# Performance work log

Measured on AMD Instinct MI355X. Metric: run time of the kernel, lower is better.

## Reference

```python
import jax, jax.numpy as jnp
import numpy as np

# dims matching init_kwargs
U, T, S, K = 2048, 200, 10, 20   # users, history_length, slate_size, num_topics
DE, DU, V, H = 32, 32, 100000, 16  # doc_embed_dim, user_embed_dim, num_docs, rnn hidden
D_IN = DE + (S + 1) + (S + 1) * K + 1  # 264 concatenated feature width
LEAKY_ALPHA = 0.3  # keras LeakyReLU default


def setup_inputs() -> dict:
    key = jax.random.key(0)
    ks = jax.random.split(key, 9)
    slate_doc_quality_history = jax.random.normal(ks[0], (U, T, S), jnp.float32)
    slate_doc_features_history = jax.random.normal(ks[1], (U, T, S, K), jnp.float32)
    docid_history = jax.random.randint(ks[2], (U, T), 0, V + 1)  # 0 is the masked id
    ctime_history = jax.random.uniform(ks[3], (U, T), jnp.float32)
    # learned parameters
    emb_table = jax.random.normal(ks[4], (V + 1, DE), jnp.float32) * 0.05
    Wx = jax.random.normal(ks[5], (D_IN, H), jnp.float32) * (1.0 / np.sqrt(D_IN))
    Wh = jax.random.normal(ks[6], (H, H), jnp.float32) * (1.0 / np.sqrt(H))
    b_rnn = jnp.zeros((H,), jnp.float32)
    Wd = jax.random.normal(ks[7], (H, DU), jnp.float32) * (1.0 / np.sqrt(H))
    b_dense = jnp.zeros((DU,), jnp.float32)
    return dict(
        slate_doc_quality_history=slate_doc_quality_history,
        slate_doc_features_history=slate_doc_features_history,
        docid_history=docid_history,
        ctime_history=ctime_history,
        emb_table=emb_table, Wx=Wx, Wh=Wh, b_rnn=b_rnn, Wd=Wd, b_dense=b_dense,
    )


def reference(slate_doc_quality_history, slate_doc_features_history, docid_history,
              ctime_history, emb_table, Wx, Wh, b_rnn, Wd, b_dense):
    B, Tlen = docid_history.shape
    # embedding lookup; mask_zero=True -> timesteps with id==0 are skipped by the RNN
    emb = emb_table[docid_history]                                   # [U,T,DE]
    mask = docid_history != 0                                        # [U,T]
    # append zero quality column -> [U,T,S+1]
    q = jnp.concatenate([slate_doc_quality_history,
                         jnp.zeros((B, Tlen, 1), slate_doc_quality_history.dtype)], axis=-1)
    # append zero feature row on slate axis, flatten -> [U,T,(S+1)*K]
    f = jnp.concatenate([slate_doc_features_history,
                         jnp.zeros((B, Tlen, 1, K), slate_doc_features_history.dtype)], axis=-2)
    f = f.reshape(B, Tlen, -1)
    x = jnp.concatenate([emb, q, f, ctime_history[..., None]], axis=-1)  # [U,T,D_IN]

    # SimpleRNN(16): h_t = tanh(x_t Wx + h_{t-1} Wh + b); masked steps keep previous h
    pre = jnp.einsum('btd,dh->bth', x, Wx) + b_rnn                   # [U,T,H]

    def step(h, inp):
        pre_t, m_t = inp                                             # [U,H], [U]
        h_new = jnp.tanh(pre_t + h @ Wh)
        h = jnp.where(m_t[:, None], h_new, h)
        return h, None

    h0 = jnp.zeros((B, Wh.shape[0]), x.dtype)
    hT, _ = jax.lax.scan(step, h0, (pre.transpose(1, 0, 2), mask.T))
    # LeakyReLU(alpha=0.3) then Dense -> user embeddings [U, DU]
    a = jnp.where(hT >= 0, hT, LEAKY_ALPHA * hT)
    return a @ Wd + b_dense
```

## Files before the change

kernel.cpp:

```cpp
#include <hip/hip_runtime.h>

#define U_   2048
#define T_   200
#define S_   10
#define K_   20
#define H_   16
#define DU_  32
#define DE_  32
#define DIN_ 264

__global__ __launch_bounds__(256) void k_pre(
    const float* __restrict__ q, const float* __restrict__ f,
    const int* __restrict__ docid, const float* __restrict__ ct,
    const float* __restrict__ emb, const float* __restrict__ Wx,
    const float* __restrict__ brnn, float* __restrict__ pre)
{
    const int idx = blockIdx.x * 256 + threadIdx.x;

    float acc[H_];
#pragma unroll
    for (int h = 0; h < H_; ++h) acc[h] = brnn[h];

    {
        const float4* f4 = (const float4*)(f + (size_t)idx * (S_ * K_));
#pragma unroll 5
        for (int r = 0; r < (S_ * K_) / 4; ++r) {
            float4 v = f4[r];
            const float* w = Wx + (DE_ + S_ + 1 + r * 4) * H_;
#pragma unroll
            for (int h = 0; h < H_; ++h)
                acc[h] += v.x * w[h] + v.y * w[h + 16] + v.z * w[h + 32] + v.w * w[h + 48];
        }
    }

    {
        const float4* e4 = (const float4*)(emb + (size_t)docid[idx] * DE_);
#pragma unroll
        for (int r = 0; r < DE_ / 4; ++r) {
            float4 v = e4[r];
            const float* w = Wx + (r * 4) * H_;
#pragma unroll
            for (int h = 0; h < H_; ++h)
                acc[h] += v.x * w[h] + v.y * w[h + 16] + v.z * w[h + 32] + v.w * w[h + 48];
        }
    }

    {
        const float2* q2 = (const float2*)(q + (size_t)idx * S_);
#pragma unroll
        for (int r = 0; r < S_ / 2; ++r) {
            float2 v = q2[r];
            const float* w = Wx + (DE_ + r * 2) * H_;
#pragma unroll
            for (int h = 0; h < H_; ++h)
                acc[h] += v.x * w[h] + v.y * w[h + 16];
        }
    }

    {
        float c = ct[idx];
        const float* w = Wx + (DIN_ - 1) * H_;
#pragma unroll
        for (int h = 0; h < H_; ++h) acc[h] += c * w[h];
    }

    float4* o = (float4*)(pre + (size_t)idx * H_);
    o[0] = make_float4(acc[0], acc[1], acc[2], acc[3]);
    o[1] = make_float4(acc[4], acc[5], acc[6], acc[7]);
    o[2] = make_float4(acc[8], acc[9], acc[10], acc[11]);
    o[3] = make_float4(acc[12], acc[13], acc[14], acc[15]);
}

__device__ __forceinline__ float tanh_fast(float x) {
    float e = __expf(2.f * x);
    return 1.f - 2.f / (e + 1.f);
}

__global__ __launch_bounds__(64) void k_rnn(
    const float* __restrict__ pre, const int* __restrict__ docid,
    const float* __restrict__ Wh, const float* __restrict__ Wd,
    const float* __restrict__ bd, float* __restrict__ out)
{
    const int tid = threadIdx.x;
    const int l = tid & 15;
    const int u = (blockIdx.x * 64 + tid) >> 4;

    const float* prow = pre + (size_t)u * T_ * H_;
    const int* drow = docid + (size_t)u * T_;

    float wh[16];
#pragma unroll
    for (int k = 0; k < 16; ++k) wh[k] = Wh[((l ^ k) << 4) | l];

    float h = 0.f;

    float pb0 = prow[0 * H_ + l], pb1 = prow[1 * H_ + l],
          pb2 = prow[2 * H_ + l], pb3 = prow[3 * H_ + l];
    int   m0 = drow[0], m1 = drow[1], m2 = drow[2], m3 = drow[3];

    for (int tb = 0; tb < T_; tb += 4) {
#pragma unroll
        for (int s = 0; s < 4; ++s) {
            float p; int m;
            if      (s == 0) { p = pb0; m = m0; }
            else if (s == 1) { p = pb1; m = m1; }
            else if (s == 2) { p = pb2; m = m2; }
            else             { p = pb3; m = m3; }

            int tn = tb + 4 + s; if (tn > T_ - 1) tn = T_ - 1;
            float pn = prow[tn * H_ + l];
            int   mn = drow[tn];
            if      (s == 0) { pb0 = pn; m0 = mn; }
            else if (s == 1) { pb1 = pn; m1 = mn; }
            else if (s == 2) { pb2 = pn; m2 = mn; }
            else             { pb3 = pn; m3 = mn; }

            float a0 = p, a1 = 0.f, a2 = 0.f, a3 = 0.f;
#pragma unroll
            for (int k = 0; k < 16; k += 4) {
                a0 += __shfl_xor(h, k + 0, 16) * wh[k + 0];
                a1 += __shfl_xor(h, k + 1, 16) * wh[k + 1];
                a2 += __shfl_xor(h, k + 2, 16) * wh[k + 2];
                a3 += __shfl_xor(h, k + 3, 16) * wh[k + 3];
            }
            float accv = (a0 + a1) + (a2 + a3);
            float th = tanh_fast(accv);
            h = (m != 0) ? th : h;
        }
    }

    float a = (h >= 0.f) ? h : 0.3f * h;

    float wd0[16], wd1[16];
#pragma unroll
    for (int k = 0; k < 16; ++k) {
        int j = l ^ k;
        wd0[k] = Wd[j * DU_ + l];
        wd1[k] = Wd[j * DU_ + l + 16];
    }
    float o0 = bd[l], o1 = bd[l + 16];
#pragma unroll
    for (int k = 0; k < 16; ++k) {
        float av = __shfl_xor(a, k, 16);
        o0 += av * wd0[k];
        o1 += av * wd1[k];
    }
    out[(size_t)u * DU_ + l] = o0;
    out[(size_t)u * DU_ + l + 16] = o1;
}

extern "C" void kernel_launch(void* const* d_in, const int* in_sizes, int n_in,
                              void* d_out, int out_size, void* d_ws, size_t ws_size,
                              hipStream_t stream) {
    const float* q     = (const float*)d_in[0];
    const float* f     = (const float*)d_in[1];
    const int*   docid = (const int*)  d_in[2];
    const float* ct    = (const float*)d_in[3];
    const float* emb   = (const float*)d_in[4];
    const float* Wx    = (const float*)d_in[5];
    const float* Wh    = (const float*)d_in[6];
    const float* brnn  = (const float*)d_in[7];
    const float* Wd    = (const float*)d_in[8];
    const float* bd    = (const float*)d_in[9];
    float* out = (float*)d_out;

    float* pre = (float*)d_ws;

    k_pre<<<(U_ * T_) / 256, 256, 0, stream>>>(q, f, docid, ct, emb, Wx, brnn, pre);
    k_rnn<<<(U_ * H_) / 64, 64, 0, stream>>>(pre, docid, Wh, Wd, bd, out);
}
```

Measured before the change: 175.2 us.

## Stage feature and quality tiles through LDS with async double-buffered global_load_lds

The projection kernel no longer has each thread read its own 800-byte feature row with strided float4 loads. The block now loads the tile cooperatively into LDS with global_load_lds, so consecutive lanes fetch contiguous 16-byte chunks, with a swizzled layout and double buffering across 13 chunks. Quality values are staged through LDS the same way. This is meant to make the feature loads coalesced and to overlap loading with the FMA work, at the cost of extra barriers, about 36 KB of LDS per block and lower occupancy.

Result: slower. 187.3 us (+6.9%).

```diff
diff --git a/kernel.cpp b/kernel.cpp
--- a/kernel.cpp
+++ b/kernel.cpp
@@ -9,29 +9,48 @@
 #define DE_  32
 #define DIN_ 264
 
-__global__ __launch_bounds__(256) void k_pre(
+#define THREADS 256
+#define TILE 256
+
+__device__ __forceinline__ void g2l16(const void* g, void* l) {
+    __builtin_amdgcn_global_load_lds(
+        (const __attribute__((address_space(1))) void*)g,
+        (__attribute__((address_space(3))) void*)l, 16, 0, 0);
+}
+
+__global__ __launch_bounds__(THREADS) void k_pre(
     const float* __restrict__ q, const float* __restrict__ f,
     const int* __restrict__ docid, const float* __restrict__ ct,
     const float* __restrict__ emb, const float* __restrict__ Wx,
     const float* __restrict__ brnn, float* __restrict__ pre)
 {
-    const int idx = blockIdx.x * 256 + threadIdx.x;
+    __shared__ __align__(16) float fbuf[2][TILE * 16];
+    __shared__ __align__(16) float qbuf[TILE * S_];
+    const int t = threadIdx.x;
+    const int tile = blockIdx.x * TILE;
+    const int idx = tile + t;
+
+    const char* fbase = (const char*)f + (size_t)tile * 800;
+
+#pragma unroll
+    for (int r = 0; r < 4; ++r) {
+        int g = r * THREADS + t;
+        int pos = g >> 2, s = g & 3;
+        int sub = s ^ ((pos >> 1) & 3);
+        g2l16(fbase + (size_t)pos * 800 + sub * 16, (char*)&fbuf[0][0] + g * 16);
+    }
+    {
+        const char* qbase = (const char*)q + (size_t)tile * 40;
+#pragma unroll
+        for (int r = 0; r < 3; ++r) {
+            int g = r * THREADS + t;
+            if (g < 640) g2l16(qbase + (size_t)g * 16, (char*)qbuf + g * 16);
+        }
+    }
 
     float acc[H_];
 #pragma unroll
     for (int h = 0; h < H_; ++h) acc[h] = brnn[h];
-
-    {
-        const float4* f4 = (const float4*)(f + (size_t)idx * (S_ * K_));
-#pragma unroll 5
-        for (int r = 0; r < (S_ * K_) / 4; ++r) {
-            float4 v = f4[r];
-            const float* w = Wx + (DE_ + S_ + 1 + r * 4) * H_;
-#pragma unroll
-            for (int h = 0; h < H_; ++h)
-                acc[h] += v.x * w[h] + v.y * w[h + 16] + v.z * w[h + 32] + v.w * w[h + 48];
-        }
-    }
 
     {
         const float4* e4 = (const float4*)(emb + (size_t)docid[idx] * DE_);
@@ -43,25 +62,72 @@
             for (int h = 0; h < H_; ++h)
                 acc[h] += v.x * w[h] + v.y * w[h + 16] + v.z * w[h + 32] + v.w * w[h + 48];
         }
+        float c = ct[idx];
+        const float* w = Wx + (DIN_ - 1) * H_;
+#pragma unroll
+        for (int h = 0; h < H_; ++h) acc[h] += c * w[h];
+    }
+
+#pragma unroll 1
+    for (int c = 0; c < 13; ++c) {
+        __syncthreads();
+        if (c < 11) {
+            char* db = (char*)&fbuf[(c + 1) & 1][0];
+#pragma unroll
+            for (int r = 0; r < 4; ++r) {
+                int g = r * THREADS + t;
+                int pos = g >> 2, s = g & 3;
+                int sub = s ^ ((pos >> 1) & 3);
+                g2l16(fbase + (size_t)pos * 800 + (c + 1) * 64 + sub * 16, db + g * 16);
+            }
+        } else if (c == 11) {
+            char* db = (char*)&fbuf[0][0];
+#pragma unroll
+            for (int r = 0; r < 2; ++r) {
+                int g = r * THREADS + t;
+                int pos = g >> 1, s = g & 1;
+                int sub = s ^ ((pos >> 2) & 1);
+                g2l16(fbase + (size_t)pos * 800 + 768 + sub * 16, db + g * 16);
+            }
+        }
+
+        if (c < 12) {
+            const float* base = &fbuf[c & 1][0];
+            const float* wc = Wx + (43 + c * 16) * H_;
+#pragma unroll
+            for (int j = 0; j < 4; ++j) {
+                int slot = j ^ ((t >> 1) & 3);
+                float4 v = *(const float4*)(base + t * 16 + slot * 4);
+                const float* w = wc + (4 * j) * H_;
+#pragma unroll
+                for (int h = 0; h < H_; ++h)
+                    acc[h] += v.x * w[h] + v.y * w[h + 16] + v.z * w[h + 32] + v.w * w[h + 48];
+            }
+        } else {
+            const float* base = &fbuf[0][0];
+            const float* wc = Wx + (43 + 192) * H_;
+#pragma unroll
+            for (int j = 0; j < 2; ++j) {
+                int slot = j ^ ((t >> 2) & 1);
+                float4 v = *(const float4*)(base + t * 8 + slot * 4);
+                const float* w = wc + (4 * j) * H_;
+#pragma unroll
+                for (int h = 0; h < H_; ++h)
+                    acc[h] += v.x * w[h] + v.y * w[h + 16] + v.z * w[h + 32] + v.w * w[h + 48];
+            }
+        }
     }
 
     {
-        const float2* q2 = (const float2*)(q + (size_t)idx * S_);
+        const float* xq = qbuf + t * S_;
 #pragma unroll
         for (int r = 0; r < S_ / 2; ++r) {
-            float2 v = q2[r];
-            const float* w = Wx + (DE_ + r * 2) * H_;
+            float2 v = *(const float2*)(xq + 2 * r);
+            const float* w = Wx + (DE_ + 2 * r) * H_;
 #pragma unroll
             for (int h = 0; h < H_; ++h)
                 acc[h] += v.x * w[h] + v.y * w[h + 16];
         }
-    }
-
-    {
-        float c = ct[idx];
-        const float* w = Wx + (DIN_ - 1) * H_;
-#pragma unroll
-        for (int h = 0; h < H_; ++h) acc[h] += c * w[h];
     }
 
     float4* o = (float4*)(pre + (size_t)idx * H_);
@@ -166,6 +232,6 @@
 
     float* pre = (float*)d_ws;
 
-    k_pre<<<(U_ * T_) / 256, 256, 0, stream>>>(q, f, docid, ct, emb, Wx, brnn, pre);
+    k_pre<<<(U_ * T_) / TILE, THREADS, 0, stream>>>(q, f, docid, ct, emb, Wx, brnn, pre);
     k_rnn<<<(U_ * H_) / 64, 64, 0, stream>>>(pre, docid, Wh, Wd, bd, out);
 }
```

## Stage feature rows through LDS with coalesced, double-buffered global loads

Applied to the files above, without the earlier changes.

k_pre now runs 64-thread blocks. Each block loads its contiguous 64×800-byte chunk of slate features with fully coalesced float4 loads, double-buffered in registers, and writes them into padded shared memory. Each thread then reads its own row from LDS for the feature dot product, while the embedding, quality and ctime contributions are computed before the barrier. This replaces the old per-thread strided 800-byte row reads, which coalesced poorly, in exchange for about 51KB of LDS per block, which limits occupancy, plus higher register pressure.

New measurement: 204.9 us. 17.0% more time.

```diff
diff --git a/kernel.cpp b/kernel.cpp
--- a/kernel.cpp
+++ b/kernel.cpp
@@ -9,59 +9,102 @@
 #define DE_  32
 #define DIN_ 264
 
-__global__ __launch_bounds__(256) void k_pre(
+#define POSB 64
+#define ROWB 800
+#define RPAD 808
+
+__global__ __launch_bounds__(64) void k_pre(
     const float* __restrict__ q, const float* __restrict__ f,
     const int* __restrict__ docid, const float* __restrict__ ct,
     const float* __restrict__ emb, const float* __restrict__ Wx,
     const float* __restrict__ brnn, float* __restrict__ pre)
 {
-    const int idx = blockIdx.x * 256 + threadIdx.x;
+    __shared__ __align__(16) char lbuf[POSB * RPAD];
+    const int t = threadIdx.x;
+    const int blk = blockIdx.x;
+    const int idx = blk * POSB + t;
+
+    const char* src = (const char*)f + (size_t)blk * (POSB * ROWB);
+
+    float4 ga[10], gb[10];
+
+#pragma unroll
+    for (int i = 0; i < 10; ++i)
+        ga[i] = *(const float4*)(src + (size_t)(i * 64 + t) * 16);
+
+    const int did = docid[idx];
+    float4 e[8];
+    const float4* e4 = (const float4*)(emb + (size_t)did * DE_);
+#pragma unroll
+    for (int r = 0; r < 8; ++r) e[r] = e4[r];
+    float2 qv[5];
+    const float2* q2 = (const float2*)(q + (size_t)idx * S_);
+#pragma unroll
+    for (int r = 0; r < 5; ++r) qv[r] = q2[r];
+    const float cv = ct[idx];
+
+#pragma unroll
+    for (int r = 0; r < 5; ++r) {
+        if (r < 4) {
+            if ((r & 1) == 0) {
+#pragma unroll
+                for (int i = 0; i < 10; ++i)
+                    gb[i] = *(const float4*)(src + (size_t)((r + 1) * 640 + i * 64 + t) * 16);
+            } else {
+#pragma unroll
+                for (int i = 0; i < 10; ++i)
+                    ga[i] = *(const float4*)(src + (size_t)((r + 1) * 640 + i * 64 + t) * 16);
+            }
+        }
+#pragma unroll
+        for (int i = 0; i < 10; ++i) {
+            const int g = r * 640 + i * 64 + t;
+            const int pos = g / 50;
+            const int off = pos * RPAD + (g - pos * 50) * 16;
+            const float4 v = ((r & 1) == 0) ? ga[i] : gb[i];
+            *(float2*)(lbuf + off)     = make_float2(v.x, v.y);
+            *(float2*)(lbuf + off + 8) = make_float2(v.z, v.w);
+        }
+    }
 
     float acc[H_];
 #pragma unroll
     for (int h = 0; h < H_; ++h) acc[h] = brnn[h];
 
+#pragma unroll
+    for (int r = 0; r < 8; ++r) {
+        const float4 v = e[r];
+        const float* w = Wx + (r * 4) * H_;
+#pragma unroll
+        for (int h = 0; h < H_; ++h)
+            acc[h] += v.x * w[h] + v.y * w[h + 16] + v.z * w[h + 32] + v.w * w[h + 48];
+    }
     {
-        const float4* f4 = (const float4*)(f + (size_t)idx * (S_ * K_));
-#pragma unroll 5
-        for (int r = 0; r < (S_ * K_) / 4; ++r) {
-            float4 v = f4[r];
-            const float* w = Wx + (DE_ + S_ + 1 + r * 4) * H_;
-#pragma unroll
-            for (int h = 0; h < H_; ++h)
-                acc[h] += v.x * w[h] + v.y * w[h + 16] + v.z * w[h + 32] + v.w * w[h + 48];
-        }
-    }
+        const float* w = Wx + (DIN_ - 1) * H_;
+#pragma unroll
+        for (int h = 0; h < H_; ++h) acc[h] += cv * w[h];
+    }
+#pragma unroll
+    for (int j = 0; j < 5; ++j) {
+        const float2 v = qv[j];
+        const float* w = Wx + (DE_ + 2 * j) * H_;
+#pragma unroll
+        for (int h = 0; h < H_; ++h)
+            acc[h] += v.x * w[h] + v.y * w[h + 16];
+    }
+
+    __syncthreads();
 
     {
-        const float4* e4 = (const float4*)(emb + (size_t)docid[idx] * DE_);
-#pragma unroll
-        for (int r = 0; r < DE_ / 4; ++r) {
-            float4 v = e4[r];
-            const float* w = Wx + (r * 4) * H_;
-#pragma unroll
-            for (int h = 0; h < H_; ++h)
-                acc[h] += v.x * w[h] + v.y * w[h + 16] + v.z * w[h + 32] + v.w * w[h + 48];
-        }
-    }
-
-    {
-        const float2* q2 = (const float2*)(q + (size_t)idx * S_);
-#pragma unroll
-        for (int r = 0; r < S_ / 2; ++r) {
-            float2 v = q2[r];
-            const float* w = Wx + (DE_ + r * 2) * H_;
+        const float2* row = (const float2*)(lbuf + t * RPAD);
+#pragma unroll 10
+        for (int k = 0; k < 100; ++k) {
+            const float2 v = row[k];
+            const float* w = Wx + (43 + 2 * k) * H_;
 #pragma unroll
             for (int h = 0; h < H_; ++h)
                 acc[h] += v.x * w[h] + v.y * w[h + 16];
         }
-    }
-
-    {
-        float c = ct[idx];
-        const float* w = Wx + (DIN_ - 1) * H_;
-#pragma unroll
-        for (int h = 0; h < H_; ++h) acc[h] += c * w[h];
     }
 
     float4* o = (float4*)(pre + (size_t)idx * H_);
@@ -166,6 +209,6 @@
 
     float* pre = (float*)d_ws;
 
-    k_pre<<<(U_ * T_) / 256, 256, 0, stream>>>(q, f, docid, ct, emb, Wx, brnn, pre);
+    k_pre<<<(U_ * T_) / POSB, POSB, 0, stream>>>(q, f, docid, ct, emb, Wx, brnn, pre);
     k_rnn<<<(U_ * H_) / 64, 64, 0, stream>>>(pre, docid, Wh, Wd, bd, out);
 }
```

## Split feature projection into persistent LDS-staged kernel with async global-to-LDS loads

Applied to the files above, without the earlier changes.

The large slate-feature part of the input projection moves into its own persistent kernel of 256 blocks. It stages 64 timestep rows at a time into swizzled LDS using double-buffered global_load_lds, and splits the 50 float4 chunks of each row across 8 waves with an LDS reduction. A second kernel handles the embedding, quality and ctime terms and accumulates into pre with a read-modify-write. The aim is coalesced, pipelined streaming of the 327MB feature tensor in place of strided per-thread float4 loads. The cost is an extra kernel launch and an extra read/write pass over pre.

After: 301.4 us. +72.0%, slower.

```diff
diff --git a/kernel.cpp b/kernel.cpp
--- a/kernel.cpp
+++ b/kernel.cpp
@@ -9,11 +9,119 @@
 #define DE_  32
 #define DIN_ 264
 
-__global__ __launch_bounds__(256) void k_pre(
-    const float* __restrict__ q, const float* __restrict__ f,
-    const int* __restrict__ docid, const float* __restrict__ ct,
-    const float* __restrict__ emb, const float* __restrict__ Wx,
-    const float* __restrict__ brnn, float* __restrict__ pre)
+#define TPOS   64
+#define GR     50
+#define GRP    56
+#define NSTW   7
+#define NBLK   256
+#define NITER  25
+
+__device__ __forceinline__ void g2l16(const void* g, void* l) {
+    __builtin_amdgcn_global_load_lds(
+        (const __attribute__((address_space(1))) void*)g,
+        (__attribute__((address_space(3))) void*)l, 16, 0, 0);
+}
+
+__global__ __launch_bounds__(512, 2) void k_pre_f(
+    const float* __restrict__ f, const float* __restrict__ Wx,
+    float* __restrict__ pre)
+{
+    __shared__ __align__(16) char fbuf[2][TPOS * GRP * 16];
+    __shared__ __align__(16) char red[TPOS * 33 * 16];
+    const int t    = threadIdx.x;
+    const int lane = t & 63;
+    const int w    = t >> 6;
+    const int b    = blockIdx.x;
+
+    const int jbase = w * 6 + (w < 2 ? w : 2);
+    const int jcnt  = (w < 2) ? 7 : 6;
+
+    int srcoff[NSTW];
+#pragma unroll
+    for (int m = 0; m < NSTW; ++m) {
+        const unsigned sp = (unsigned)(t + 512 * m);
+        const unsigned p  = sp / GRP;
+        unsigned j = (sp - p * GRP) ^ (p & 7u);
+        if (j >= GR) j = 0;
+        srcoff[m] = (int)(p * 800u + j * 16u);
+    }
+
+    const char* fB = (const char*)f;
+    const int pp = lane & 7;
+    const int rp = t >> 3;
+    const int hp = t & 7;
+
+    {
+        const char* src = fB + (size_t)b * 51200;
+        char* dst = (char*)fbuf[0];
+#pragma unroll
+        for (int m = 0; m < NSTW; ++m)
+            g2l16(src + srcoff[m], dst + (size_t)(t + 512 * m) * 16);
+    }
+
+#pragma unroll 1
+    for (int i = 0; i < NITER; ++i) {
+        const int cur = i & 1;
+        if (i + 1 < NITER) {
+            const char* src = fB + (size_t)((i + 1) * NBLK + b) * 51200;
+            char* dst = (char*)fbuf[cur ^ 1];
+#pragma unroll
+            for (int m = 0; m < NSTW; ++m)
+                g2l16(src + srcoff[m], dst + (size_t)(t + 512 * m) * 16);
+        }
+        __builtin_amdgcn_sched_barrier(0);
+        if (i + 1 < NITER) asm volatile("s_waitcnt vmcnt(7)" ::: "memory");
+        else               asm volatile("s_waitcnt vmcnt(0)" ::: "memory");
+        __builtin_amdgcn_s_barrier();
+        __builtin_amdgcn_sched_barrier(0);
+
+        const char* fb = (const char*)fbuf[cur];
+        float acc[H_];
+#pragma unroll
+        for (int h = 0; h < H_; ++h) acc[h] = 0.f;
+#pragma unroll
+        for (int k = 0; k < 7; ++k) {
+            if (k < jcnt) {
+                const int j = jbase + k;
+                const int slot = lane * GRP + (j ^ pp);
+                const float4 v = *(const float4*)(fb + (size_t)slot * 16);
+                const float* wt = Wx + (43 + 4 * j) * H_;
+#pragma unroll
+                for (int h = 0; h < H_; ++h)
+                    acc[h] += v.x * wt[h] + v.y * wt[h + 16]
+                            + v.z * wt[h + 32] + v.w * wt[h + 48];
+            }
+        }
+
+        {
+            char* rb = red + (size_t)(lane * 33 + w * 4) * 16;
+            *(float4*)(rb +  0) = make_float4(acc[0],  acc[1],  acc[2],  acc[3]);
+            *(float4*)(rb + 16) = make_float4(acc[4],  acc[5],  acc[6],  acc[7]);
+            *(float4*)(rb + 32) = make_float4(acc[8],  acc[9],  acc[10], acc[11]);
+            *(float4*)(rb + 48) = make_float4(acc[12], acc[13], acc[14], acc[15]);
+        }
+        asm volatile("s_waitcnt lgkmcnt(0)" ::: "memory");
+        __builtin_amdgcn_s_barrier();
+        __builtin_amdgcn_sched_barrier(0);
+
+        {
+            float sx = 0.f, sy = 0.f;
+#pragma unroll
+            for (int o = 0; o < 8; ++o) {
+                const float2 v = *(const float2*)(red + (size_t)(rp * 33 + o * 4) * 16 + hp * 8);
+                sx += v.x; sy += v.y;
+            }
+            const int tile = i * NBLK + b;
+            *(float2*)(pre + ((size_t)tile * TPOS + rp) * H_ + hp * 2) = make_float2(sx, sy);
+        }
+    }
+}
+
+__global__ __launch_bounds__(256) void k_emb(
+    const float* __restrict__ q, const int* __restrict__ docid,
+    const float* __restrict__ ct, const float* __restrict__ emb,
+    const float* __restrict__ Wx, const float* __restrict__ brnn,
+    float* __restrict__ pre)
 {
     const int idx = blockIdx.x * 256 + threadIdx.x;
 
@@ -22,53 +130,40 @@
     for (int h = 0; h < H_; ++h) acc[h] = brnn[h];
 
     {
-        const float4* f4 = (const float4*)(f + (size_t)idx * (S_ * K_));
-#pragma unroll 5
-        for (int r = 0; r < (S_ * K_) / 4; ++r) {
-            float4 v = f4[r];
-            const float* w = Wx + (DE_ + S_ + 1 + r * 4) * H_;
+        const float4* e4 = (const float4*)(emb + (size_t)docid[idx] * DE_);
+#pragma unroll
+        for (int r = 0; r < DE_ / 4; ++r) {
+            const float4 v = e4[r];
+            const float* wt = Wx + (r * 4) * H_;
 #pragma unroll
             for (int h = 0; h < H_; ++h)
-                acc[h] += v.x * w[h] + v.y * w[h + 16] + v.z * w[h + 32] + v.w * w[h + 48];
-        }
-    }
-
-    {
-        const float4* e4 = (const float4*)(emb + (size_t)docid[idx] * DE_);
-#pragma unroll
-        for (int r = 0; r < DE_ / 4; ++r) {
-            float4 v = e4[r];
-            const float* w = Wx + (r * 4) * H_;
+                acc[h] += v.x * wt[h] + v.y * wt[h + 16] + v.z * wt[h + 32] + v.w * wt[h + 48];
+        }
+    }
+    {
+        const float2* q2 = (const float2*)(q + (size_t)idx * S_);
+#pragma unroll
+        for (int r = 0; r < S_ / 2; ++r) {
+            const float2 v = q2[r];
+            const float* wt = Wx + (DE_ + 2 * r) * H_;
 #pragma unroll
             for (int h = 0; h < H_; ++h)
-                acc[h] += v.x * w[h] + v.y * w[h + 16] + v.z * w[h + 32] + v.w * w[h + 48];
-        }
-    }
-
-    {
-        const float2* q2 = (const float2*)(q + (size_t)idx * S_);
-#pragma unroll
-        for (int r = 0; r < S_ / 2; ++r) {
-            float2 v = q2[r];
-            const float* w = Wx + (DE_ + r * 2) * H_;
-#pragma unroll
-            for (int h = 0; h < H_; ++h)
-                acc[h] += v.x * w[h] + v.y * w[h + 16];
-        }
-    }
-
-    {
-        float c = ct[idx];
-        const float* w = Wx + (DIN_ - 1) * H_;
-#pragma unroll
-        for (int h = 0; h < H_; ++h) acc[h] += c * w[h];
+                acc[h] += v.x * wt[h] + v.y * wt[h + 16];
+        }
+    }
+    {
+        const float c = ct[idx];
+        const float* wt = Wx + (DIN_ - 1) * H_;
+#pragma unroll
+        for (int h = 0; h < H_; ++h) acc[h] += c * wt[h];
     }
 
     float4* o = (float4*)(pre + (size_t)idx * H_);
-    o[0] = make_float4(acc[0], acc[1], acc[2], acc[3]);
-    o[1] = make_float4(acc[4], acc[5], acc[6], acc[7]);
-    o[2] = make_float4(acc[8], acc[9], acc[10], acc[11]);
-    o[3] = make_float4(acc[12], acc[13], acc[14], acc[15]);
+    float4 p0 = o[0], p1 = o[1], p2 = o[2], p3 = o[3];
+    o[0] = make_float4(p0.x + acc[0],  p0.y + acc[1],  p0.z + acc[2],  p0.w + acc[3]);
+    o[1] = make_float4(p1.x + acc[4],  p1.y + acc[5],  p1.z + acc[6],  p1.w + acc[7]);
+    o[2] = make_float4(p2.x + acc[8],  p2.y + acc[9],  p2.z + acc[10], p2.w + acc[11]);
+    o[3] = make_float4(p3.x + acc[12], p3.y + acc[13], p3.z + acc[14], p3.w + acc[15]);
 }
 
 __device__ __forceinline__ float tanh_fast(float x) {
@@ -166,6 +261,7 @@
 
     float* pre = (float*)d_ws;
 
-    k_pre<<<(U_ * T_) / 256, 256, 0, stream>>>(q, f, docid, ct, emb, Wx, brnn, pre);
+    k_pre_f<<<NBLK, 512, 0, stream>>>(f, Wx, pre);
+    k_emb<<<(U_ * T_) / 256, 256, 0, stream>>>(q, docid, ct, emb, Wx, brnn, pre);
     k_rnn<<<(U_ * H_) / 64, 64, 0, stream>>>(pre, docid, Wh, Wd, bd, out);
 }
```
